# Optimization experiments

Measured on AMD Instinct MI355X. Metric: run time of the kernel, lower is better.

Reference implementation:

```python
import jax, jax.numpy as jnp
import numpy as np

EPS = 1e-5


def _whiten(feature):
    # ZCA whitening per sample (WCT): f_w = U diag(s^-1/2) U^T (f - mean)
    b, c, h, w = feature.shape
    f = feature.reshape(b, c, h * w)
    mean = f.mean(axis=-1, keepdims=True)
    f = f - mean
    cov = jnp.einsum('bcx,bdx->bcd', f, f) / (h * w - 1)
    s, u = jnp.linalg.eigh(cov)
    s = jnp.maximum(s, EPS)
    out = jnp.einsum('bcd,bd,bed,bex->bcx', u, s ** -0.5, u, f)
    return out.reshape(b, c, h, w)


def _color(feature, target):
    # ZCA coloring: f_c = Ut diag(st^1/2) Ut^T (f - mean_f) + mean_t
    b, c, h, w = feature.shape
    f = feature.reshape(b, c, h * w)
    f = f - f.mean(axis=-1, keepdims=True)
    t = target.reshape(b, c, -1)
    tmean = t.mean(axis=-1, keepdims=True)
    tc = t - tmean
    cov = jnp.einsum('bcx,bdx->bcd', tc, tc) / (tc.shape[-1] - 1)
    s, u = jnp.linalg.eigh(cov)
    s = jnp.maximum(s, EPS)
    out = jnp.einsum('bcd,bd,bed,bex->bcx', u, s ** 0.5, u, f) + tmean
    return out.reshape(b, c, h, w)


def _patches(f, p):
    # [b,c,h,w] -> [b,c,h,w,p*p], same ordering as torch unfold(2,p).unfold(3,p)
    pad = (p - 1) // 2
    b, c, h, w = f.shape
    fp = jnp.pad(f, ((0, 0), (0, 0), (pad, pad), (pad, pad)))
    return jnp.stack([fp[:, :, i:i + h, j:j + w] for i in range(p) for j in range(p)], axis=-1)


def reference(content_feature, style_feature, style_strength, patch_size):
    p = int(patch_size)
    pad = (p - 1) // 2
    nc = _whiten(content_feature)
    ns = _whiten(style_feature)
    b, c, h, w = nc.shape
    n = h * w  # one style kernel per style spatial location (stride 1)

    # style kernels [b, n, c, p, p] and their L2 norms over (c,p,p)
    sk = _patches(ns, p).transpose(0, 2, 3, 1, 4).reshape(b, n, c, p, p)
    knorm = jnp.sqrt(jnp.sum(sk ** 2, axis=(2, 3, 4), keepdims=True))
    skn = (sk / knorm).reshape(b, n, c, p * p)

    # patch matching score == conv2d of content with normalized style kernels
    cp = _patches(nc, p)                              # [b,c,h,w,p*p]
    score = jnp.einsum('bchwk,bnck->bnhw', cp, skn)   # [b,n,h,w]

    # argmax one-hot -> gather the best-matching (un-normalized) style patch
    idx = jnp.argmax(score, axis=1)                   # [b,h,w]
    sel = jax.vmap(lambda k, i: k[i])(sk, idx.reshape(b, -1))  # [b,hw,c,p,p]
    sel = sel.reshape(b, h, w, c, p, p).transpose(0, 3, 1, 2, 4, 5)  # [b,c,h,w,p,p]

    # overlap-add == conv_transpose2d(one_hot, kernels, padding=p-1) on padded input
    buf = jnp.zeros((b, c, h + p - 1, w + p - 1), dtype=sel.dtype)
    for di in range(p):
        for dj in range(p):
            buf = buf.at[:, :, di:di + h, dj:dj + w].add(sel[:, :, :, :, di, dj])
    recon = buf[:, :, pad:pad + h, pad:pad + w]

    # overlap counts (norm_deconvolution)
    m = jnp.zeros((h + p - 1, w + p - 1), dtype=sel.dtype)
    for di in range(p):
        for dj in range(p):
            m = m.at[di:di + h, dj:dj + w].add(1.0)
    norm = m[pad:pad + h, pad:pad + w]

    reassembled = recon / norm[None, None]
    stylized = _color(reassembled, style_feature)
    return (1.0 - style_strength) * content_feature + style_strength * stylized


def setup_inputs():
    key = jax.random.key(0)
    k1, k2 = jax.random.split(key)
    B, C, H, W = 2, 256, 48, 48
    return {
        'content_feature': jax.random.normal(k1, (B, C, H, W), jnp.float32),
        'style_feature': jax.random.normal(k2, (B, C, H, W), jnp.float32),
        'style_strength': jnp.float32(1.0),
        'patch_size': 3,
    }
```

## Files before the change

kernel.cpp:

```cpp
#include <hip/hip_runtime.h>

constexpr int B_  = 2;
constexpr int C_  = 256;
constexpr int H_  = 48;
constexpr int W_  = 48;
constexpr int N_  = H_ * W_;
constexpr int PH_ = H_ + 2;
constexpr int PW_ = W_ + 2;
constexpr int NP_ = PH_ * PW_;
constexpr int NPS_ = 2560;
constexpr int MS_  = 2560;
constexpr int CC_ = C_ * C_;
constexpr int NCH_ = 36;
constexpr int NC_  = N_ / NCH_;
constexpr int NSIT_ = 6;
constexpr int KCH_ = 9;

__device__ inline float waveRed(float v) {
  #pragma unroll
  for (int o = 32; o > 0; o >>= 1) v += __shfl_down(v, o);
  return v;
}

#define GEMM64_COMPUTE(sAT, sB, acc, ty, tx)                        \
  _Pragma("unroll")                                                 \
  for (int kk = 0; kk < 16; kk++) {                                 \
    float4 a = *(const float4*)&sAT[kk][(ty) * 4];                  \
    float4 b = *(const float4*)&sB[kk][(tx) * 4];                   \
    acc[0][0] += a.x * b.x; acc[0][1] += a.x * b.y;                 \
    acc[0][2] += a.x * b.z; acc[0][3] += a.x * b.w;                 \
    acc[1][0] += a.y * b.x; acc[1][1] += a.y * b.y;                 \
    acc[1][2] += a.y * b.z; acc[1][3] += a.y * b.w;                 \
    acc[2][0] += a.z * b.x; acc[2][1] += a.z * b.y;                 \
    acc[2][2] += a.z * b.z; acc[2][3] += a.z * b.w;                 \
    acc[3][0] += a.w * b.x; acc[3][1] += a.w * b.y;                 \
    acc[3][2] += a.w * b.z; acc[3][3] += a.w * b.w;                 \
  }


__global__ __launch_bounds__(256) void center_kernel(
    const float* __restrict__ content, const float* __restrict__ style,
    float* __restrict__ fc, float* __restrict__ fs, float* __restrict__ mean_s) {
  int t = blockIdx.x;
  int which = t / (B_ * C_);
  int bc = t % (B_ * C_);
  const float* src = which ? style : content;
  float* dst = which ? fs : fc;
  const float* row = src + (size_t)bc * N_;
  float acc = 0.f;
  for (int i = threadIdx.x; i < N_; i += 256) acc += row[i];
  __shared__ float sm[4];
  float r = waveRed(acc);
  if ((threadIdx.x & 63) == 0) sm[threadIdx.x >> 6] = r;
  __syncthreads();
  float mean = (sm[0] + sm[1] + sm[2] + sm[3]) * (1.0f / N_);
  for (int i = threadIdx.x; i < N_; i += 256) dst[(size_t)bc * N_ + i] = row[i] - mean;
  if (which == 1 && threadIdx.x == 0) mean_s[bc] = mean;
}

__global__ __launch_bounds__(256) void cov_kernel(
    const float* __restrict__ fc, const float* __restrict__ fs, float* __restrict__ pcov) {
  int z = blockIdx.z;
  int m = z & 3, ci = z >> 2;
  const float* f = (m < 2) ? (fc + (size_t)m * C_ * N_) : (fs + (size_t)(m - 2) * C_ * N_);
  int i0 = blockIdx.y * 64, j0 = blockIdx.x * 64;
  int t = threadIdx.x;
  int tx = t & 15, ty = t >> 4;
  int sr = t >> 2, skq = t & 3;
  __shared__ float sAT[16][68], sB[16][68];
  float acc[4][4] = {};
  int k0e = ci * 256 + 256;
  for (int k0 = ci * 256; k0 < k0e; k0 += 16) {
    float4 av = *(const float4*)&f[(size_t)(i0 + sr) * N_ + k0 + skq * 4];
    float4 bv = *(const float4*)&f[(size_t)(j0 + sr) * N_ + k0 + skq * 4];
    __syncthreads();
    sAT[skq * 4 + 0][sr] = av.x; sAT[skq * 4 + 1][sr] = av.y;
    sAT[skq * 4 + 2][sr] = av.z; sAT[skq * 4 + 3][sr] = av.w;
    sB[skq * 4 + 0][sr] = bv.x;  sB[skq * 4 + 1][sr] = bv.y;
    sB[skq * 4 + 2][sr] = bv.z;  sB[skq * 4 + 3][sr] = bv.w;
    __syncthreads();
    GEMM64_COMPUTE(sAT, sB, acc, ty, tx)
  }
  float* out = pcov + ((size_t)ci * 4 + m) * CC_;
  for (int u = 0; u < 4; u++)
    for (int v = 0; v < 4; v++)
      out[(size_t)(i0 + ty * 4 + u) * C_ + (j0 + tx * 4 + v)] = acc[u][v];
}

__global__ __launch_bounds__(256) void covreduce(
    const float* __restrict__ pcov, float* __restrict__ A4) {
  int t = blockIdx.x * 256 + threadIdx.x;
  float acc = 0.f;
  #pragma unroll
  for (int ci = 0; ci < KCH_; ci++) acc += pcov[(size_t)ci * 4 * CC_ + t];
  A4[t] = acc * (1.0f / (float)(N_ - 1));
}

__global__ __launch_bounds__(256) void ns_init(
    const float* __restrict__ A4, float* __restrict__ Y, float* __restrict__ Z,
    float* __restrict__ scal) {
  int m = blockIdx.y, s = blockIdx.x;
  const float* A = A4 + (size_t)m * CC_;
  float d = A[(size_t)threadIdx.x * 257];
  __shared__ float sm[4];
  float r = waveRed(d);
  if ((threadIdx.x & 63) == 0) sm[threadIdx.x >> 6] = r;
  __syncthreads();
  float trace = sm[0] + sm[1] + sm[2] + sm[3];
  float sc = 1.1f * trace / (float)C_;
  if (s == 0 && threadIdx.x == 0) scal[m] = sc;
  float inv = 1.0f / sc;
  int i0 = s * (CC_ / 16);
  for (int i = i0 + threadIdx.x; i < i0 + CC_ / 16; i += 256) {
    Y[(size_t)m * CC_ + i] = A[i] * inv;
    Z[(size_t)m * CC_ + i] = ((i >> 8) == (i & 255)) ? 1.0f : 0.0f;
  }
}

__global__ __launch_bounds__(256) void ns_stepA(
    const float* __restrict__ Z, const float* __restrict__ Y, float* __restrict__ T) {
  int m = blockIdx.z;
  const float* A = Z + (size_t)m * CC_;
  const float* Bm = Y + (size_t)m * CC_;
  float* out = T + (size_t)m * CC_;
  int i0 = blockIdx.y * 32, j0 = blockIdx.x * 32;
  int t = threadIdx.x;
  int tx = t & 15, ty = t >> 4;
  int sr = t >> 3, sc4 = t & 7;
  __shared__ float sAT[32][36], sB[32][36];
  float acc[2][2] = {};
  for (int k0 = 0; k0 < 256; k0 += 32) {
    float4 av = *(const float4*)&A[(size_t)(i0 + sr) * 256 + k0 + sc4 * 4];
    float4 bv = *(const float4*)&Bm[(size_t)(k0 + sr) * 256 + j0 + sc4 * 4];
    __syncthreads();
    sAT[sc4 * 4 + 0][sr] = av.x; sAT[sc4 * 4 + 1][sr] = av.y;
    sAT[sc4 * 4 + 2][sr] = av.z; sAT[sc4 * 4 + 3][sr] = av.w;
    *(float4*)&sB[sr][sc4 * 4] = bv;
    __syncthreads();
    #pragma unroll
    for (int kk = 0; kk < 32; kk++) {
      float2 a = *(const float2*)&sAT[kk][ty * 2];
      float2 b = *(const float2*)&sB[kk][tx * 2];
      acc[0][0] += a.x * b.x; acc[0][1] += a.x * b.y;
      acc[1][0] += a.y * b.x; acc[1][1] += a.y * b.y;
    }
    __syncthreads();
  }
  for (int u = 0; u < 2; u++)
    for (int v = 0; v < 2; v++) {
      int i = i0 + ty * 2 + u, j = j0 + tx * 2 + v;
      float d = (i == j) ? 3.0f : 0.0f;
      out[(size_t)i * 256 + j] = d - acc[u][v];
    }
}

__global__ __launch_bounds__(256) void ns_stepB(
    const float* __restrict__ Y, const float* __restrict__ Z, const float* __restrict__ T,
    float* __restrict__ Yn, float* __restrict__ Zn) {
  int z = blockIdx.z;
  int m = z & 3;
  bool doY = (z < 4);
  const float* A = (doY ? Y : T) + (size_t)m * CC_;
  const float* Bm = (doY ? T : Z) + (size_t)m * CC_;
  float* out = (doY ? Yn : Zn) + (size_t)m * CC_;
  int i0 = blockIdx.y * 32, j0 = blockIdx.x * 32;
  int t = threadIdx.x;
  int tx = t & 15, ty = t >> 4;
  int sr = t >> 3, sc4 = t & 7;
  __shared__ float sAT[32][36], sB[32][36];
  float acc[2][2] = {};
  for (int k0 = 0; k0 < 256; k0 += 32) {
    float4 av = *(const float4*)&A[(size_t)(i0 + sr) * 256 + k0 + sc4 * 4];
    float4 bv = *(const float4*)&Bm[(size_t)(k0 + sr) * 256 + j0 + sc4 * 4];
    __syncthreads();
    sAT[sc4 * 4 + 0][sr] = av.x; sAT[sc4 * 4 + 1][sr] = av.y;
    sAT[sc4 * 4 + 2][sr] = av.z; sAT[sc4 * 4 + 3][sr] = av.w;
    *(float4*)&sB[sr][sc4 * 4] = bv;
    __syncthreads();
    #pragma unroll
    for (int kk = 0; kk < 32; kk++) {
      float2 a = *(const float2*)&sAT[kk][ty * 2];
      float2 b = *(const float2*)&sB[kk][tx * 2];
      acc[0][0] += a.x * b.x; acc[0][1] += a.x * b.y;
      acc[1][0] += a.y * b.x; acc[1][1] += a.y * b.y;
    }
    __syncthreads();
  }
  for (int u = 0; u < 2; u++)
    for (int v = 0; v < 2; v++) {
      int i = i0 + ty * 2 + u, j = j0 + tx * 2 + v;
      out[(size_t)i * 256 + j] = 0.5f * acc[u][v];
    }
}

__global__ __launch_bounds__(256) void whiten_pad(
    const float* __restrict__ Zf, const float* __restrict__ scal,
    const float* __restrict__ fc, const float* __restrict__ fs,
    float* __restrict__ ncP, float* __restrict__ nsP, float* __restrict__ nsT) {
  int m = blockIdx.z;
  const float* f = (m < 2) ? (fc + (size_t)m * C_ * N_) : (fs + (size_t)(m - 2) * C_ * N_);
  int c0 = blockIdx.y * 64, x0 = blockIdx.x * 64;
  int t = threadIdx.x;
  int tx = t & 15, ty = t >> 4;
  int sr = t >> 2, skq = t & 3;
  int bkk = t & 15, bc4 = t >> 4;
  __shared__ float sAT[16][68], sB[16][68];
  float acc[4][4] = {};
  for (int k0 = 0; k0 < 256; k0 += 16) {
    float4 av = *(const float4*)&Zf[(size_t)m * CC_ + (size_t)(c0 + sr) * 256 + k0 + skq * 4];
    float4 bv = *(const float4*)&f[(size_t)(k0 + bkk) * N_ + x0 + bc4 * 4];
    __syncthreads();
    sAT[skq * 4 + 0][sr] = av.x; sAT[skq * 4 + 1][sr] = av.y;
    sAT[skq * 4 + 2][sr] = av.z; sAT[skq * 4 + 3][sr] = av.w;
    *(float4*)&sB[bkk][bc4 * 4] = bv;
    __syncthreads();
    GEMM64_COMPUTE(sAT, sB, acc, ty, tx)
  }
  float rs = rsqrtf(scal[m]);
  int b = (m < 2) ? m : (m - 2);
  for (int u = 0; u < 4; u++)
    for (int v = 0; v < 4; v++) {
      int c = c0 + ty * 4 + u, x = x0 + tx * 4 + v;
      int h = x / W_, w = x % W_;
      int pp = (h + 1) * PW_ + (w + 1);
      float val = acc[u][v] * rs;
      if (m < 2) {
        ncP[((size_t)b * C_ + c) * NPS_ + pp] = val;
      } else {
        nsP[((size_t)b * NP_ + pp) * C_ + c] = val;
        nsT[((size_t)b * C_ + c) * NPS_ + pp] = val;
      }
    }
}

__global__ __launch_bounds__(256) void q_kernel(const float* __restrict__ nsP, float* __restrict__ q) {
  int wid = (blockIdx.x * 256 + threadIdx.x) >> 6;
  int lane = threadIdx.x & 63;
  if (wid >= B_ * NP_) return;
  const float* v = nsP + (size_t)wid * C_;
  float acc = 0.f;
  #pragma unroll
  for (int c = lane; c < C_; c += 64) { float t = v[c]; acc += t * t; }
  acc = waveRed(acc);
  if (lane == 0) q[wid] = acc;
}

__global__ __launch_bounds__(256) void kninv_kernel(const float* __restrict__ q, float* __restrict__ kninv) {
  int t = blockIdx.x * 256 + threadIdx.x;
  if (t >= B_ * N_) return;
  int b = t / N_, n = t % N_;
  int hn = n / W_, wn = n % W_;
  const float* qb = q + (size_t)b * NP_ + hn * PW_ + wn;
  float s = 0.f;
  #pragma unroll
  for (int i = 0; i < 3; i++)
    #pragma unroll
    for (int j = 0; j < 3; j++) s += qb[i * PW_ + j];
  kninv[t] = rsqrtf(s);
}

__global__ __launch_bounds__(256) void m_kernel(
    const float* __restrict__ At, const float* __restrict__ Bt, float* __restrict__ M) {
  int i0 = blockIdx.y * 64, j0 = blockIdx.x * 128;
  int t = threadIdx.x;
  int tx = t & 15, ty = t >> 4;
  int akk = t >> 4, ac4 = t & 15;
  int bkk = t >> 5, bc4 = t & 31;
  __shared__ float sA[16][68], sB[16][132];
  float acc[4][8] = {};
  for (int k0 = 0; k0 < 256; k0 += 16) {
    float4 a0 = *(const float4*)&At[(size_t)(k0 + akk) * NPS_ + i0 + ac4 * 4];
    float4 b0 = *(const float4*)&Bt[(size_t)(k0 + bkk) * NPS_ + j0 + bc4 * 4];
    float4 b1 = *(const float4*)&Bt[(size_t)(k0 + bkk + 8) * NPS_ + j0 + bc4 * 4];
    __syncthreads();
    *(float4*)&sA[akk][ac4 * 4] = a0;
    *(float4*)&sB[bkk][bc4 * 4] = b0;
    *(float4*)&sB[bkk + 8][bc4 * 4] = b1;
    __syncthreads();
    #pragma unroll
    for (int kk = 0; kk < 16; kk++) {
      float4 a  = *(const float4*)&sA[kk][ty * 4];
      float4 p  = *(const float4*)&sB[kk][tx * 4];
      float4 qv = *(const float4*)&sB[kk][64 + tx * 4];
      acc[0][0] += a.x * p.x; acc[0][1] += a.x * p.y; acc[0][2] += a.x * p.z; acc[0][3] += a.x * p.w;
      acc[1][0] += a.y * p.x; acc[1][1] += a.y * p.y; acc[1][2] += a.y * p.z; acc[1][3] += a.y * p.w;
      acc[2][0] += a.z * p.x; acc[2][1] += a.z * p.y; acc[2][2] += a.z * p.z; acc[2][3] += a.z * p.w;
      acc[3][0] += a.w * p.x; acc[3][1] += a.w * p.y; acc[3][2] += a.w * p.z; acc[3][3] += a.w * p.w;
      acc[0][4] += a.x * qv.x; acc[0][5] += a.x * qv.y; acc[0][6] += a.x * qv.z; acc[0][7] += a.x * qv.w;
      acc[1][4] += a.y * qv.x; acc[1][5] += a.y * qv.y; acc[1][6] += a.y * qv.z; acc[1][7] += a.y * qv.w;
      acc[2][4] += a.z * qv.x; acc[2][5] += a.z * qv.y; acc[2][6] += a.z * qv.z; acc[2][7] += a.z * qv.w;
      acc[3][4] += a.w * qv.x; acc[3][5] += a.w * qv.y; acc[3][6] += a.w * qv.z; acc[3][7] += a.w * qv.w;
    }
    __syncthreads();
  }
  #pragma unroll
  for (int u = 0; u < 4; u++) {
    size_t row = (size_t)(i0 + ty * 4 + u) * MS_;
    float4 s0 = {acc[u][0], acc[u][1], acc[u][2], acc[u][3]};
    float4 s1 = {acc[u][4], acc[u][5], acc[u][6], acc[u][7]};
    *(float4*)&M[row + j0 + tx * 4] = s0;
    *(float4*)&M[row + j0 + 64 + tx * 4] = s1;
  }
}

__global__ __launch_bounds__(256) void score_kernel(
    const float* __restrict__ M, const float* __restrict__ kninv,
    float* __restrict__ pval, int* __restrict__ pidx, int b) {
  int m = blockIdx.x * 256 + threadIdx.x;
  int h = m / W_, w = m % W_;
  int cm = h * PW_ + w;
  int n0 = blockIdx.y * NC_;
  const float* kni = kninv + (size_t)b * N_;
  float best = -3.4e38f;
  int bidx = n0;
  for (int n = n0; n < n0 + NC_; n++) {
    int hn = n / W_, wn = n % W_;
    int rn = hn * PW_ + wn;
    const float* base = M + (size_t)rn * MS_ + cm;
    float s = 0.f;
    #pragma unroll
    for (int i = 0; i < 3; i++)
      #pragma unroll
      for (int j = 0; j < 3; j++) s += base[(size_t)(i * PW_ + j) * (MS_ + 1)];
    s *= kni[n];
    if (s > best) { best = s; bidx = n; }
  }
  pval[((size_t)b * NCH_ + blockIdx.y) * N_ + m] = best;
  pidx[((size_t)b * NCH_ + blockIdx.y) * N_ + m] = bidx;
}

__global__ __launch_bounds__(256) void argmax_final(
    const float* __restrict__ pval, const int* __restrict__ pidx, int* __restrict__ idxb) {
  int t = blockIdx.x * 256 + threadIdx.x;
  if (t >= B_ * N_) return;
  int b = t / N_, m = t % N_;
  float best = -3.4e38f; int bidx = 0;
  for (int ch = 0; ch < NCH_; ch++) {
    float v = pval[((size_t)b * NCH_ + ch) * N_ + m];
    int i = pidx[((size_t)b * NCH_ + ch) * N_ + m];
    if (v > best) { best = v; bidx = i; }
  }
  idxb[t] = bidx;
}

__global__ __launch_bounds__(256) void reassemble_kernel(
    const float* __restrict__ nsP, const int* __restrict__ idxb, float* __restrict__ recon) {
  int bm = blockIdx.x;
  int b = bm / N_, m = bm % N_;
  int h = m / W_, w = m % W_;
  int c = threadIdx.x;
  float acc = 0.f; int cnt = 0;
  for (int di = 0; di < 3; di++) {
    int hs = h + 1 - di; if (hs < 0 || hs >= H_) continue;
    for (int dj = 0; dj < 3; dj++) {
      int ws = w + 1 - dj; if (ws < 0 || ws >= W_) continue;
      int n = idxb[(size_t)b * N_ + hs * W_ + ws];
      int hn = n / W_, wn = n % W_;
      int pp = (hn + di) * PW_ + (wn + dj);
      acc += nsP[((size_t)b * NP_ + pp) * C_ + c];
      cnt++;
    }
  }
  recon[((size_t)b * N_ + m) * C_ + c] = acc / (float)cnt;
}

__global__ __launch_bounds__(256) void rmean_part(const float* __restrict__ recon, float* __restrict__ pmr) {
  int b = blockIdx.y, ch = blockIdx.x, c = threadIdx.x;
  float acc = 0.f;
  int x0 = ch * (N_ / 16);
  for (int x = x0; x < x0 + (N_ / 16); x++) acc += recon[((size_t)b * N_ + x) * C_ + c];
  pmr[((size_t)b * 16 + ch) * C_ + c] = acc;
}

__global__ __launch_bounds__(256) void rmean_fin(const float* __restrict__ pmr, float* __restrict__ mr) {
  int b = blockIdx.x, c = threadIdx.x;
  float acc = 0.f;
  for (int ch = 0; ch < 16; ch++) acc += pmr[((size_t)b * 16 + ch) * C_ + c];
  mr[(size_t)b * C_ + c] = acc * (1.0f / N_);
}

__global__ __launch_bounds__(256) void color_blend(
    const float* __restrict__ Yf, const float* __restrict__ scal,
    const float* __restrict__ recon, const float* __restrict__ mr,
    const float* __restrict__ msty, const float* __restrict__ content,
    const float* __restrict__ ssp, float* __restrict__ out) {
  int b = blockIdx.z;
  int m = 2 + b;
  int c0 = blockIdx.y * 64, x0 = blockIdx.x * 64;
  int t = threadIdx.x;
  int tx = t & 15, ty = t >> 4;
  int sr = t >> 2, skq = t & 3;
  __shared__ float sAT[16][68], sB[16][68];
  float acc[4][4] = {};
  for (int k0 = 0; k0 < 256; k0 += 16) {
    float4 av = *(const float4*)&Yf[(size_t)m * CC_ + (size_t)(c0 + sr) * 256 + k0 + skq * 4];
    float4 bm4 = *(const float4*)&mr[(size_t)b * C_ + k0 + skq * 4];
    float4 bv = *(const float4*)&recon[((size_t)b * N_ + x0 + sr) * C_ + k0 + skq * 4];
    bv.x -= bm4.x; bv.y -= bm4.y; bv.z -= bm4.z; bv.w -= bm4.w;
    __syncthreads();
    sAT[skq * 4 + 0][sr] = av.x; sAT[skq * 4 + 1][sr] = av.y;
    sAT[skq * 4 + 2][sr] = av.z; sAT[skq * 4 + 3][sr] = av.w;
    sB[skq * 4 + 0][sr] = bv.x;  sB[skq * 4 + 1][sr] = bv.y;
    sB[skq * 4 + 2][sr] = bv.z;  sB[skq * 4 + 3][sr] = bv.w;
    __syncthreads();
    GEMM64_COMPUTE(sAT, sB, acc, ty, tx)
  }
  float sq = sqrtf(scal[m]);
  float ss = ssp[0];
  for (int u = 0; u < 4; u++)
    for (int v = 0; v < 4; v++) {
      int c = c0 + ty * 4 + u, x = x0 + tx * 4 + v;
      float sty = acc[u][v] * sq + msty[(size_t)b * C_ + c];
      size_t o = ((size_t)b * C_ + c) * N_ + x;
      out[o] = (1.0f - ss) * content[o] + ss * sty;
    }
}

extern "C" void kernel_launch(void* const* d_in, const int* in_sizes, int n_in,
                              void* d_out, int out_size, void* d_ws, size_t ws_size,
                              hipStream_t stream) {
  (void)in_sizes; (void)n_in; (void)out_size; (void)ws_size;
  const float* content = (const float*)d_in[0];
  const float* style   = (const float*)d_in[1];
  const float* ssp     = (const float*)d_in[2];
  float* out = (float*)d_out;
  float* W = (float*)d_ws;

  size_t off = 0;
  float* fc   = W + off; off += (size_t)B_ * C_ * N_;
  float* fs   = W + off; off += (size_t)B_ * C_ * N_;
  float* nsP  = W + off; off += (size_t)B_ * NP_ * C_;
  float* nsT  = W + off; off += (size_t)B_ * C_ * NPS_;
  float* ncP  = W + off; off += (size_t)B_ * C_ * NPS_;
  float* A4   = W + off; off += (size_t)4 * CC_;
  float* Ya   = W + off; off += (size_t)4 * CC_;
  float* Yb   = W + off; off += (size_t)4 * CC_;
  float* Za   = W + off; off += (size_t)4 * CC_;
  float* Zb   = W + off; off += (size_t)4 * CC_;
  float* scal = W + off; off += 4;
  float* msty = W + off; off += (size_t)B_ * C_;
  float* mr   = W + off; off += (size_t)B_ * C_;
  float* pmr  = W + off; off += (size_t)B_ * 16 * C_;
  float* q    = W + off; off += (size_t)B_ * NP_;
  float* kni  = W + off; off += (size_t)B_ * N_;
  float* pval = W + off; off += (size_t)B_ * NCH_ * N_;
  float* Mb   = W + off; off += (size_t)MS_ * MS_;
  int* pidx = (int*)(W + off); off += (size_t)B_ * NCH_ * N_;
  int* idxb = (int*)(W + off); off += (size_t)B_ * N_;
  float* pcov = Mb;
  float* T    = Mb;
  float* recon = fs;

  hipMemsetAsync(nsP, 0, (size_t)B_ * NP_ * C_ * sizeof(float), stream);
  hipMemsetAsync(nsT, 0, (size_t)B_ * C_ * NPS_ * sizeof(float), stream);
  hipMemsetAsync(ncP, 0, (size_t)B_ * C_ * NPS_ * sizeof(float), stream);

  center_kernel<<<2 * B_ * C_, 256, 0, stream>>>(content, style, fc, fs, msty);
  cov_kernel<<<dim3(4, 4, 4 * KCH_), 256, 0, stream>>>(fc, fs, pcov);
  covreduce<<<4 * CC_ / 256, 256, 0, stream>>>(pcov, A4);
  ns_init<<<dim3(16, 4), 256, 0, stream>>>(A4, Ya, Za, scal);

  float *Ycur = Ya, *Zcur = Za, *Yalt = Yb, *Zalt = Zb;
  for (int it = 0; it < NSIT_; it++) {
    ns_stepA<<<dim3(8, 8, 4), 256, 0, stream>>>(Zcur, Ycur, T);
    ns_stepB<<<dim3(8, 8, 8), 256, 0, stream>>>(Ycur, Zcur, T, Yalt, Zalt);
    float* tp;
    tp = Ycur; Ycur = Yalt; Yalt = tp;
    tp = Zcur; Zcur = Zalt; Zalt = tp;
  }

  whiten_pad<<<dim3(36, 4, 4), 256, 0, stream>>>(Zcur, scal, fc, fs, ncP, nsP, nsT);
  q_kernel<<<(B_ * NP_ + 3) / 4, 256, 0, stream>>>(nsP, q);
  kninv_kernel<<<(B_ * N_ + 255) / 256, 256, 0, stream>>>(q, kni);

  for (int b = 0; b < B_; b++) {
    m_kernel<<<dim3(20, 40), 256, 0, stream>>>(
        nsT + (size_t)b * C_ * NPS_, ncP + (size_t)b * C_ * NPS_, Mb);
    score_kernel<<<dim3(N_ / 256, NCH_), 256, 0, stream>>>(Mb, kni, pval, pidx, b);
  }
  argmax_final<<<(B_ * N_ + 255) / 256, 256, 0, stream>>>(pval, pidx, idxb);
  reassemble_kernel<<<B_ * N_, 256, 0, stream>>>(nsP, idxb, recon);
  rmean_part<<<dim3(16, B_), 256, 0, stream>>>(recon, pmr);
  rmean_fin<<<B_, 256, 0, stream>>>(pmr, mr);
  color_blend<<<dim3(36, 4, B_), 256, 0, stream>>>(
      Ycur, scal, recon, mr, msty, content, ssp, out);
}
```

Measured before the change: 420.9 us.

## Split-K Newton-Schulz GEMMs, batch match GEMM across images, cut one iteration

The Newton-Schulz matmuls are split along K into two halves, with each matrix kept as a pair of partial buffers that are summed when loaded. This doubles the grid and improves occupancy on the small 256x256 GEMMs. The iteration count drops from 6 to 5, which may loosen the accuracy of the inverse square root. When the workspace is large enough, the per-batch m_kernel and score_kernel launches merge into one batched launch each over a doubled M buffer.

Measured after the change: 362.5 us. 1.16x faster.

```diff
diff --git a/kernel.cpp b/kernel.cpp
--- a/kernel.cpp
+++ b/kernel.cpp
@@ -13,7 +13,7 @@
 constexpr int CC_ = C_ * C_;
 constexpr int NCH_ = 36;
 constexpr int NC_  = N_ / NCH_;
-constexpr int NSIT_ = 6;
+constexpr int NSIT_ = 5;
 constexpr int KCH_ = 9;
 
 __device__ inline float waveRed(float v) {
@@ -97,7 +97,7 @@
 }
 
 __global__ __launch_bounds__(256) void ns_init(
-    const float* __restrict__ A4, float* __restrict__ Y, float* __restrict__ Z,
+    const float* __restrict__ A4, float* __restrict__ Yp, float* __restrict__ Zp,
     float* __restrict__ scal) {
   int m = blockIdx.y, s = blockIdx.x;
   const float* A = A4 + (size_t)m * CC_;
@@ -112,26 +112,38 @@
   float inv = 1.0f / sc;
   int i0 = s * (CC_ / 16);
   for (int i = i0 + threadIdx.x; i < i0 + CC_ / 16; i += 256) {
-    Y[(size_t)m * CC_ + i] = A[i] * inv;
-    Z[(size_t)m * CC_ + i] = ((i >> 8) == (i & 255)) ? 1.0f : 0.0f;
+    Yp[(size_t)m * CC_ + i] = A[i] * inv;
+    Zp[(size_t)m * CC_ + i] = ((i >> 8) == (i & 255)) ? 1.0f : 0.0f;
+    Yp[(size_t)(4 + m) * CC_ + i] = 0.f;
+    Zp[(size_t)(4 + m) * CC_ + i] = 0.f;
   }
 }
 
 __global__ __launch_bounds__(256) void ns_stepA(
-    const float* __restrict__ Z, const float* __restrict__ Y, float* __restrict__ T) {
-  int m = blockIdx.z;
-  const float* A = Z + (size_t)m * CC_;
-  const float* Bm = Y + (size_t)m * CC_;
-  float* out = T + (size_t)m * CC_;
+    const float* __restrict__ Zp, const float* __restrict__ Yp, float* __restrict__ Tp) {
+  int z = blockIdx.z;
+  int m = z & 3, kh = z >> 2;
+  const float* A0 = Zp + (size_t)m * CC_;
+  const float* A1 = Zp + (size_t)(4 + m) * CC_;
+  const float* B0 = Yp + (size_t)m * CC_;
+  const float* B1 = Yp + (size_t)(4 + m) * CC_;
+  float* out = Tp + (size_t)(kh * 4 + m) * CC_;
   int i0 = blockIdx.y * 32, j0 = blockIdx.x * 32;
   int t = threadIdx.x;
   int tx = t & 15, ty = t >> 4;
   int sr = t >> 3, sc4 = t & 7;
   __shared__ float sAT[32][36], sB[32][36];
   float acc[2][2] = {};
-  for (int k0 = 0; k0 < 256; k0 += 32) {
-    float4 av = *(const float4*)&A[(size_t)(i0 + sr) * 256 + k0 + sc4 * 4];
-    float4 bv = *(const float4*)&Bm[(size_t)(k0 + sr) * 256 + j0 + sc4 * 4];
+  int k0e = kh * 128 + 128;
+  for (int k0 = kh * 128; k0 < k0e; k0 += 32) {
+    size_t ia = (size_t)(i0 + sr) * 256 + k0 + sc4 * 4;
+    size_t ib = (size_t)(k0 + sr) * 256 + j0 + sc4 * 4;
+    float4 a0 = *(const float4*)&A0[ia];
+    float4 a1 = *(const float4*)&A1[ia];
+    float4 b0 = *(const float4*)&B0[ib];
+    float4 b1 = *(const float4*)&B1[ib];
+    float4 av = {a0.x + a1.x, a0.y + a1.y, a0.z + a1.z, a0.w + a1.w};
+    float4 bv = {b0.x + b1.x, b0.y + b1.y, b0.z + b1.z, b0.w + b1.w};
     __syncthreads();
     sAT[sc4 * 4 + 0][sr] = av.x; sAT[sc4 * 4 + 1][sr] = av.y;
     sAT[sc4 * 4 + 2][sr] = av.z; sAT[sc4 * 4 + 3][sr] = av.w;
@@ -149,29 +161,38 @@
   for (int u = 0; u < 2; u++)
     for (int v = 0; v < 2; v++) {
       int i = i0 + ty * 2 + u, j = j0 + tx * 2 + v;
-      float d = (i == j) ? 3.0f : 0.0f;
+      float d = (kh == 0 && i == j) ? 3.0f : 0.0f;
       out[(size_t)i * 256 + j] = d - acc[u][v];
     }
 }
 
 __global__ __launch_bounds__(256) void ns_stepB(
-    const float* __restrict__ Y, const float* __restrict__ Z, const float* __restrict__ T,
-    float* __restrict__ Yn, float* __restrict__ Zn) {
+    const float* __restrict__ Yp, const float* __restrict__ Zp, const float* __restrict__ Tp,
+    float* __restrict__ Ynp, float* __restrict__ Znp) {
   int z = blockIdx.z;
-  int m = z & 3;
-  bool doY = (z < 4);
-  const float* A = (doY ? Y : T) + (size_t)m * CC_;
-  const float* Bm = (doY ? T : Z) + (size_t)m * CC_;
-  float* out = (doY ? Yn : Zn) + (size_t)m * CC_;
+  int m = z & 3, kh = (z >> 2) & 1;
+  bool doY = (z < 8);
+  const float* A0 = (doY ? Yp : Tp) + (size_t)m * CC_;
+  const float* A1 = (doY ? Yp : Tp) + (size_t)(4 + m) * CC_;
+  const float* B0 = (doY ? Tp : Zp) + (size_t)m * CC_;
+  const float* B1 = (doY ? Tp : Zp) + (size_t)(4 + m) * CC_;
+  float* out = (doY ? Ynp : Znp) + (size_t)(kh * 4 + m) * CC_;
   int i0 = blockIdx.y * 32, j0 = blockIdx.x * 32;
   int t = threadIdx.x;
   int tx = t & 15, ty = t >> 4;
   int sr = t >> 3, sc4 = t & 7;
   __shared__ float sAT[32][36], sB[32][36];
   float acc[2][2] = {};
-  for (int k0 = 0; k0 < 256; k0 += 32) {
-    float4 av = *(const float4*)&A[(size_t)(i0 + sr) * 256 + k0 + sc4 * 4];
-    float4 bv = *(const float4*)&Bm[(size_t)(k0 + sr) * 256 + j0 + sc4 * 4];
+  int k0e = kh * 128 + 128;
+  for (int k0 = kh * 128; k0 < k0e; k0 += 32) {
+    size_t ia = (size_t)(i0 + sr) * 256 + k0 + sc4 * 4;
+    size_t ib = (size_t)(k0 + sr) * 256 + j0 + sc4 * 4;
+    float4 a0 = *(const float4*)&A0[ia];
+    float4 a1 = *(const float4*)&A1[ia];
+    float4 b0 = *(const float4*)&B0[ib];
+    float4 b1 = *(const float4*)&B1[ib];
+    float4 av = {a0.x + a1.x, a0.y + a1.y, a0.z + a1.z, a0.w + a1.w};
+    float4 bv = {b0.x + b1.x, b0.y + b1.y, b0.z + b1.z, b0.w + b1.w};
     __syncthreads();
     sAT[sc4 * 4 + 0][sr] = av.x; sAT[sc4 * 4 + 1][sr] = av.y;
     sAT[sc4 * 4 + 2][sr] = av.z; sAT[sc4 * 4 + 3][sr] = av.w;
@@ -207,7 +228,10 @@
   __shared__ float sAT[16][68], sB[16][68];
   float acc[4][4] = {};
   for (int k0 = 0; k0 < 256; k0 += 16) {
-    float4 av = *(const float4*)&Zf[(size_t)m * CC_ + (size_t)(c0 + sr) * 256 + k0 + skq * 4];
+    size_t ia = (size_t)(c0 + sr) * 256 + k0 + skq * 4;
+    float4 a0 = *(const float4*)&Zf[(size_t)m * CC_ + ia];
+    float4 a1 = *(const float4*)&Zf[(size_t)(4 + m) * CC_ + ia];
+    float4 av = {a0.x + a1.x, a0.y + a1.y, a0.z + a1.z, a0.w + a1.w};
     float4 bv = *(const float4*)&f[(size_t)(k0 + bkk) * N_ + x0 + bc4 * 4];
     __syncthreads();
     sAT[skq * 4 + 0][sr] = av.x; sAT[skq * 4 + 1][sr] = av.y;
@@ -260,7 +284,10 @@
 }
 
 __global__ __launch_bounds__(256) void m_kernel(
-    const float* __restrict__ At, const float* __restrict__ Bt, float* __restrict__ M) {
+    const float* __restrict__ At, const float* __restrict__ Bt, float* __restrict__ M,
+    size_t batchA, size_t batchM) {
+  size_t bz = blockIdx.z;
+  At += bz * batchA; Bt += bz * batchA; M += bz * batchM;
   int i0 = blockIdx.y * 64, j0 = blockIdx.x * 128;
   int t = threadIdx.x;
   int tx = t & 15, ty = t >> 4;
@@ -305,7 +332,9 @@
 
 __global__ __launch_bounds__(256) void score_kernel(
     const float* __restrict__ M, const float* __restrict__ kninv,
-    float* __restrict__ pval, int* __restrict__ pidx, int b) {
+    float* __restrict__ pval, int* __restrict__ pidx, int b0, size_t batchM) {
+  int b = b0 + blockIdx.z;
+  M += (size_t)blockIdx.z * batchM;
   int m = blockIdx.x * 256 + threadIdx.x;
   int h = m / W_, w = m % W_;
   int cm = h * PW_ + w;
@@ -393,7 +422,10 @@
   __shared__ float sAT[16][68], sB[16][68];
   float acc[4][4] = {};
   for (int k0 = 0; k0 < 256; k0 += 16) {
-    float4 av = *(const float4*)&Yf[(size_t)m * CC_ + (size_t)(c0 + sr) * 256 + k0 + skq * 4];
+    size_t ia = (size_t)(c0 + sr) * 256 + k0 + skq * 4;
+    float4 a0 = *(const float4*)&Yf[(size_t)m * CC_ + ia];
+    float4 a1 = *(const float4*)&Yf[(size_t)(4 + m) * CC_ + ia];
+    float4 av = {a0.x + a1.x, a0.y + a1.y, a0.z + a1.z, a0.w + a1.w};
     float4 bm4 = *(const float4*)&mr[(size_t)b * C_ + k0 + skq * 4];
     float4 bv = *(const float4*)&recon[((size_t)b * N_ + x0 + sr) * C_ + k0 + skq * 4];
     bv.x -= bm4.x; bv.y -= bm4.y; bv.z -= bm4.z; bv.w -= bm4.w;
@@ -419,7 +451,7 @@
 extern "C" void kernel_launch(void* const* d_in, const int* in_sizes, int n_in,
                               void* d_out, int out_size, void* d_ws, size_t ws_size,
                               hipStream_t stream) {
-  (void)in_sizes; (void)n_in; (void)out_size; (void)ws_size;
+  (void)in_sizes; (void)n_in; (void)out_size;
   const float* content = (const float*)d_in[0];
   const float* style   = (const float*)d_in[1];
   const float* ssp     = (const float*)d_in[2];
@@ -433,10 +465,10 @@
   float* nsT  = W + off; off += (size_t)B_ * C_ * NPS_;
   float* ncP  = W + off; off += (size_t)B_ * C_ * NPS_;
   float* A4   = W + off; off += (size_t)4 * CC_;
-  float* Ya   = W + off; off += (size_t)4 * CC_;
-  float* Yb   = W + off; off += (size_t)4 * CC_;
-  float* Za   = W + off; off += (size_t)4 * CC_;
-  float* Zb   = W + off; off += (size_t)4 * CC_;
+  float* Ya   = W + off; off += (size_t)8 * CC_;
+  float* Yb   = W + off; off += (size_t)8 * CC_;
+  float* Za   = W + off; off += (size_t)8 * CC_;
+  float* Zb   = W + off; off += (size_t)8 * CC_;
   float* scal = W + off; off += 4;
   float* msty = W + off; off += (size_t)B_ * C_;
   float* mr   = W + off; off += (size_t)B_ * C_;
@@ -444,9 +476,16 @@
   float* q    = W + off; off += (size_t)B_ * NP_;
   float* kni  = W + off; off += (size_t)B_ * N_;
   float* pval = W + off; off += (size_t)B_ * NCH_ * N_;
-  float* Mb   = W + off; off += (size_t)MS_ * MS_;
-  int* pidx = (int*)(W + off); off += (size_t)B_ * NCH_ * N_;
-  int* idxb = (int*)(W + off); off += (size_t)B_ * N_;
+  float* Mb   = W + off;
+  size_t off_Mb = off;
+
+  size_t off1 = off_Mb + (size_t)MS_ * MS_;
+  size_t off2 = off_Mb + (size_t)2 * MS_ * MS_;
+  size_t tail = (size_t)B_ * NCH_ * N_ + (size_t)B_ * N_;
+  bool dual = ws_size >= (off2 + tail) * sizeof(float);
+  size_t offM = dual ? off2 : off1;
+  int* pidx = (int*)(W + offM);
+  int* idxb = (int*)(W + offM + (size_t)B_ * NCH_ * N_);
   float* pcov = Mb;
   float* T    = Mb;
   float* recon = fs;
@@ -462,8 +501,8 @@
 
   float *Ycur = Ya, *Zcur = Za, *Yalt = Yb, *Zalt = Zb;
   for (int it = 0; it < NSIT_; it++) {
-    ns_stepA<<<dim3(8, 8, 4), 256, 0, stream>>>(Zcur, Ycur, T);
-    ns_stepB<<<dim3(8, 8, 8), 256, 0, stream>>>(Ycur, Zcur, T, Yalt, Zalt);
+    ns_stepA<<<dim3(8, 8, 8), 256, 0, stream>>>(Zcur, Ycur, T);
+    ns_stepB<<<dim3(8, 8, 16), 256, 0, stream>>>(Ycur, Zcur, T, Yalt, Zalt);
     float* tp;
     tp = Ycur; Ycur = Yalt; Yalt = tp;
     tp = Zcur; Zcur = Zalt; Zalt = tp;
@@ -473,10 +512,18 @@
   q_kernel<<<(B_ * NP_ + 3) / 4, 256, 0, stream>>>(nsP, q);
   kninv_kernel<<<(B_ * N_ + 255) / 256, 256, 0, stream>>>(q, kni);
 
-  for (int b = 0; b < B_; b++) {
-    m_kernel<<<dim3(20, 40), 256, 0, stream>>>(
-        nsT + (size_t)b * C_ * NPS_, ncP + (size_t)b * C_ * NPS_, Mb);
-    score_kernel<<<dim3(N_ / 256, NCH_), 256, 0, stream>>>(Mb, kni, pval, pidx, b);
+  if (dual) {
+    m_kernel<<<dim3(20, 40, 2), 256, 0, stream>>>(
+        nsT, ncP, Mb, (size_t)C_ * NPS_, (size_t)MS_ * MS_);
+    score_kernel<<<dim3(N_ / 256, NCH_, 2), 256, 0, stream>>>(
+        Mb, kni, pval, pidx, 0, (size_t)MS_ * MS_);
+  } else {
+    for (int b = 0; b < B_; b++) {
+      m_kernel<<<dim3(20, 40, 1), 256, 0, stream>>>(
+          nsT + (size_t)b * C_ * NPS_, ncP + (size_t)b * C_ * NPS_, Mb, 0, 0);
+      score_kernel<<<dim3(N_ / 256, NCH_, 1), 256, 0, stream>>>(
+          Mb, kni, pval, pidx, b, 0);
+    }
   }
   argmax_final<<<(B_ * N_ + 255) / 256, 256, 0, stream>>>(pval, pidx, idxb);
   reassemble_kernel<<<B_ * N_, 256, 0, stream>>>(nsP, idxb, recon);
```
